# Kernel tuning notes

Measured on AMD Instinct MI355X. Metric: run time of the kernel, lower is better.

## Reference

```python
import jax, jax.numpy as jnp
import numpy as np

N_NODES = 100000
N_EDGES = 1600000
D_IN = 128
UNITS = 128


def setup_inputs() -> dict:
    key = jax.random.key(0)
    k1, k2, k3, k4, k5 = jax.random.split(key, 5)
    x = jax.random.normal(k1, (N_NODES, D_IN), dtype=jnp.float32)
    # glorot-uniform-like dense weight
    limit = float(np.sqrt(6.0 / (D_IN + UNITS)))
    w = jax.random.uniform(k2, (D_IN, UNITS), minval=-limit, maxval=limit, dtype=jnp.float32)
    # COO sparse adjacency: A[row, col] = val
    edge_row = jax.random.randint(k3, (N_EDGES,), 0, N_NODES, dtype=jnp.int32)
    edge_col = jax.random.randint(k4, (N_EDGES,), 0, N_NODES, dtype=jnp.int32)
    edge_val = jax.random.uniform(k5, (N_EDGES,), dtype=jnp.float32)
    return {"x": x, "w": w, "edge_row": edge_row, "edge_col": edge_col, "edge_val": edge_val}


def reference(x, w, edge_row, edge_col, edge_val):
    # dropout rate = 0.0 -> identity (module default)
    xw = x @ w                                   # [N, units] dense projection
    # sparse adjacency propagation: out[i] = sum_e val[e] * xw[col[e]] for row[e]==i
    msgs = xw[edge_col] * edge_val[:, None]      # [E, units] irregular gather
    out = jax.ops.segment_sum(msgs, edge_row, num_segments=x.shape[0])
    return jax.nn.relu(out)                      # activation
```

## Files before the change

kernel.cpp:

```cpp
#include <hip/hip_runtime.h>

#define N_NODES 100000
#define N_EDGES 1600000
#define D 128
#define NB 391
#define BCAP 4608
#define BSTRIDE 16
#define CHUNK 4000
#define NSCAT 400

typedef __attribute__((ext_vector_type(8))) short  short8;
typedef __attribute__((ext_vector_type(4))) float  floatx4;

__device__ __forceinline__ ushort f2bf(float f) {
    unsigned u = __float_as_uint(f);
    u += 0x7FFF + ((u >> 16) & 1);
    return (ushort)(u >> 16);
}
__device__ __forceinline__ float bf2f(ushort s) {
    return __uint_as_float((unsigned)s << 16);
}

__global__ __launch_bounds__(256) void gemm_xw_mfma(const float* __restrict__ x,
                                                    const float* __restrict__ w,
                                                    ushort* __restrict__ xwb) {
    __shared__ ushort wt[128 * 128];
    const int tid  = threadIdx.x;
    const int wv   = tid >> 6;
    const int lane = tid & 63;
    const int m    = lane & 15;
    const int q    = lane >> 4;

    {
        const float4* w4 = (const float4*)w;
        for (int i = tid; i < 4096; i += 256) {
            const float4 v = w4[i];
            const int k = i >> 5;
            const int n = (i & 31) << 2;
            const int c = k >> 3, kc = k & 7;
#pragma unroll
            for (int d = 0; d < 4; ++d) {
                const float val = (d == 0) ? v.x : (d == 1) ? v.y : (d == 2) ? v.z : v.w;
                const int nn = n + d;
                wt[(nn << 7) | (((c ^ (nn & 15)) & 15) << 3) | kc] = f2bf(val);
            }
        }
    }
    __syncthreads();

    const int rbase = blockIdx.x * 64 + wv * 16;
    if (rbase >= N_NODES) return;

    const float* xrow = x + (size_t)(rbase + m) * D;

    floatx4 acc[8];
#pragma unroll
    for (int t = 0; t < 8; ++t) acc[t] = (floatx4){0.f, 0.f, 0.f, 0.f};

#pragma unroll
    for (int kk = 0; kk < D; kk += 32) {
        const float4 a0 = *(const float4*)(xrow + kk + q * 8);
        const float4 a1 = *(const float4*)(xrow + kk + q * 8 + 4);
        short8 a;
        a[0] = (short)f2bf(a0.x); a[1] = (short)f2bf(a0.y);
        a[2] = (short)f2bf(a0.z); a[3] = (short)f2bf(a0.w);
        a[4] = (short)f2bf(a1.x); a[5] = (short)f2bf(a1.y);
        a[6] = (short)f2bf(a1.z); a[7] = (short)f2bf(a1.w);

#pragma unroll
        for (int t = 0; t < 8; ++t) {
            const int n  = t * 16 + m;
            const int cc = (((kk >> 3) + q) ^ m) & 15;
            const short8 b = *(const short8*)&wt[(n << 7) | (cc << 3)];
            acc[t] = __builtin_amdgcn_mfma_f32_16x16x32_bf16(a, b, acc[t], 0, 0, 0);
        }
    }

#pragma unroll
    for (int t = 0; t < 8; ++t) {
#pragma unroll
        for (int r = 0; r < 4; ++r) {
            xwb[(size_t)(rbase + q * 4 + r) * D + t * 16 + m] = f2bf(acc[t][r]);
        }
    }
}

__global__ __launch_bounds__(256) void bucket_scatter(const int* __restrict__ erow,
                                                      const int* __restrict__ ecol,
                                                      const float* __restrict__ eval,
                                                      int* __restrict__ bcnt,
                                                      int2* __restrict__ bkt) {
    __shared__ int  sA[512];
    __shared__ int  sB[512];
    __shared__ int  lcur[NB];
    __shared__ int  gbase[NB];
    __shared__ int2 stage[CHUNK];
    const int t  = threadIdx.x;
    const int e0 = blockIdx.x * CHUNK;

    sA[t] = 0; sA[t + 256] = 0;
    __syncthreads();

    for (int i = t; i < CHUNK; i += 256) {
        const int r = erow[e0 + i];
        atomicAdd(&sA[r >> 8], 1);
    }
    __syncthreads();

    int cur = 0;
    int* bufs[2] = {sA, sB};
#pragma unroll
    for (int o = 1; o < 512; o <<= 1) {
        const int* src = bufs[cur];
        int*       dst = bufs[cur ^ 1];
        const int i0 = t, i1 = t + 256;
        dst[i0] = src[i0] + ((i0 >= o) ? src[i0 - o] : 0);
        dst[i1] = src[i1] + ((i1 >= o) ? src[i1 - o] : 0);
        cur ^= 1;
        __syncthreads();
    }
    {
        const int* incl = bufs[cur];
        int*       excl = bufs[cur ^ 1];
        excl[t]       = (t == 0) ? 0 : incl[t - 1];
        excl[t + 256] = incl[t + 255];
    }
    __syncthreads();
    int* L = bufs[cur ^ 1];

    for (int b = t; b < NB; b += 256) {
        lcur[b] = L[b];
        const int cnt = L[b + 1] - L[b];
        gbase[b] = (cnt > 0) ? atomicAdd(&bcnt[b * BSTRIDE], cnt) : 0;
    }
    __syncthreads();

    for (int i = t; i < CHUNK; i += 256) {
        const int   r = erow[e0 + i];
        const int   c = ecol[e0 + i];
        const float v = eval[e0 + i];
        const int   b = r >> 8;
        const int pos = atomicAdd(&lcur[b], 1);
        stage[pos] = make_int2(((r & 255) << 17) | c, __float_as_int(v));
    }
    __syncthreads();

    for (int i = t; i < CHUNK; i += 256) {
        int lo = 0, hi = NB - 1;
        while (lo < hi) {
            const int mid = (lo + hi + 1) >> 1;
            if (L[mid] <= i) lo = mid; else hi = mid - 1;
        }
        const int b   = lo;
        const int dst = gbase[b] + (i - L[b]);
        if (dst < BCAP) bkt[(size_t)b * BCAP + dst] = stage[i];
    }
}

__global__ __launch_bounds__(512) void scan_partials(const int* __restrict__ bcnt,
                                                     int* __restrict__ part) {
    __shared__ int buf[2][512];
    const int t = threadIdx.x;
    const int v = (t < NB) ? min(bcnt[t * BSTRIDE], BCAP) : 0;
    buf[0][t] = v;
    __syncthreads();
    int cur = 0;
#pragma unroll
    for (int o = 1; o < 512; o <<= 1) {
        const int nv = buf[cur][t] + ((t >= o) ? buf[cur][t - o] : 0);
        buf[cur ^ 1][t] = nv;
        cur ^= 1;
        __syncthreads();
    }
    if (t < NB) part[t] = buf[cur][t] - v;
}

__global__ __launch_bounds__(256) void bucket_to_csr(const int* __restrict__ bcnt,
                                                     const int* __restrict__ part,
                                                     const int2* __restrict__ bkt,
                                                     int* __restrict__ off,
                                                     int2* __restrict__ csr_cv) {
    __shared__ int sA[256], sB[256], lcur[256];
    const int b = blockIdx.x;
    const int t = threadIdx.x;
    const int n = min(bcnt[b * BSTRIDE], BCAP);
    const int2* src = bkt + (size_t)b * BCAP;
    const int base = part[b];

    sA[t] = 0;
    __syncthreads();
    for (int i = t; i < n; i += 256) {
        atomicAdd(&sA[((unsigned)src[i].x) >> 17], 1);
    }
    __syncthreads();
    int cur = 0;
    int* bufs[2] = {sA, sB};
#pragma unroll
    for (int o = 1; o < 256; o <<= 1) {
        const int* s = bufs[cur];
        int*       d = bufs[cur ^ 1];
        d[t] = s[t] + ((t >= o) ? s[t - o] : 0);
        cur ^= 1;
        __syncthreads();
    }
    const int excl = (t == 0) ? 0 : bufs[cur][t - 1];
    const int gr = (b << 8) + t;
    if (gr <= N_NODES) off[gr] = base + excl;
    lcur[t] = base + excl;
    __syncthreads();

    for (int i = t; i < n; i += 256) {
        const int2 e = src[i];
        const int  rl = ((unsigned)e.x) >> 17;
        const int pos = atomicAdd(&lcur[rl], 1);
        csr_cv[pos] = make_int2(e.x & 0x1FFFF, e.y);
    }
}

__global__ __launch_bounds__(256) void gather_kernel(const int* __restrict__ off,
                                                     const int2* __restrict__ csr_cv,
                                                     const ushort* __restrict__ xwb,
                                                     float* __restrict__ out) {
    const int node = blockIdx.x * 4 + (threadIdx.x >> 6);
    const int l    = threadIdx.x & 63;
    if (node >= N_NODES) return;
    const int q  = l >> 4;
    const int lc = (l & 15) << 3;

    int       j   = off[node] + q;
    const int end = off[node + 1];

    float acc0[8] = {0, 0, 0, 0, 0, 0, 0, 0};
    float acc1[8] = {0, 0, 0, 0, 0, 0, 0, 0};

    for (; j + 4 < end; j += 8) {
        const int2 cva = csr_cv[j];
        const int2 cvb = csr_cv[j + 4];
        const short8 ma = *(const short8*)&xwb[(size_t)cva.x * D + lc];
        const short8 mb = *(const short8*)&xwb[(size_t)cvb.x * D + lc];
        const float va = __int_as_float(cva.y);
        const float vb = __int_as_float(cvb.y);
#pragma unroll
        for (int i = 0; i < 8; ++i) {
            acc0[i] += va * bf2f((ushort)ma[i]);
            acc1[i] += vb * bf2f((ushort)mb[i]);
        }
    }
    if (j < end) {
        const int2 cv = csr_cv[j];
        const short8 m = *(const short8*)&xwb[(size_t)cv.x * D + lc];
        const float v = __int_as_float(cv.y);
#pragma unroll
        for (int i = 0; i < 8; ++i) acc0[i] += v * bf2f((ushort)m[i]);
    }

#pragma unroll
    for (int i = 0; i < 8; ++i) {
        float s = acc0[i] + acc1[i];
        s += __shfl_down(s, 32);
        s += __shfl_down(s, 16);
        acc0[i] = fmaxf(s, 0.f);
    }

    if (q == 0) {
        float4 o0 = make_float4(acc0[0], acc0[1], acc0[2], acc0[3]);
        float4 o1 = make_float4(acc0[4], acc0[5], acc0[6], acc0[7]);
        float* o = out + (size_t)node * D + lc;
        *(float4*)(o + 0) = o0;
        *(float4*)(o + 4) = o1;
    }
}

extern "C" void kernel_launch(void* const* d_in, const int* in_sizes, int n_in,
                              void* d_out, int out_size, void* d_ws, size_t ws_size,
                              hipStream_t stream) {
    const float* x    = (const float*)d_in[0];
    const float* w    = (const float*)d_in[1];
    const int*   erow = (const int*)d_in[2];
    const int*   ecol = (const int*)d_in[3];
    const float* eval = (const float*)d_in[4];
    float*       out  = (float*)d_out;

    char*   ws_base = (char*)d_ws;
    ushort* xwb    = (ushort*)ws_base;
    int*    bcnt   = (int*)(ws_base + 25600000);
    int*    off    = (int*)(ws_base + 25625024);
    int*    part   = (int*)(ws_base + 26025040);
    int2*   bkt    = (int2*)(ws_base + 26026608);
    int2*   csr_cv = (int2*)(ws_base + 40440432);

    hipMemsetAsync(bcnt, 0, 25024, stream);

    gemm_xw_mfma<<<(N_NODES + 63) / 64, 256, 0, stream>>>(x, w, xwb);
    bucket_scatter<<<NSCAT, 256, 0, stream>>>(erow, ecol, eval, bcnt, bkt);
    scan_partials<<<1, 512, 0, stream>>>(bcnt, part);
    bucket_to_csr<<<NB, 256, 0, stream>>>(bcnt, part, bkt, off, csr_cv);
    gather_kernel<<<(N_NODES + 3) / 4, 256, 0, stream>>>(off, csr_cv, xwb, out);
}
```

Before: 255.5 us.

## Fuse GEMM with bucket scatter, stage buckets in LDS, widen gather unroll

Merges the GEMM and edge-bucketing kernels into one launch by splitting on block index, so the two independent stages run concurrently and one launch is dropped. The scatter stores each staged element's bucket id instead of binary-searching for it. The CSR-build kernel copies its bucket into LDS once rather than reading global memory twice. The gather loop is unrolled to four independent edges per iteration for more memory-level parallelism, and output stores become nontemporal. The shared-memory union grows LDS per block, which may lower occupancy for the GEMM blocks.

```diff
diff --git a/kernel.cpp b/kernel.cpp
--- a/kernel.cpp
+++ b/kernel.cpp
@@ -8,6 +8,7 @@
 #define BSTRIDE 16
 #define CHUNK 4000
 #define NSCAT 400
+#define NGEMM 1563
 
 typedef __attribute__((ext_vector_type(8))) short  short8;
 typedef __attribute__((ext_vector_type(4))) float  floatx4;
@@ -21,139 +22,149 @@
     return __uint_as_float((unsigned)s << 16);
 }
 
-__global__ __launch_bounds__(256) void gemm_xw_mfma(const float* __restrict__ x,
-                                                    const float* __restrict__ w,
-                                                    ushort* __restrict__ xwb) {
-    __shared__ ushort wt[128 * 128];
-    const int tid  = threadIdx.x;
-    const int wv   = tid >> 6;
-    const int lane = tid & 63;
-    const int m    = lane & 15;
-    const int q    = lane >> 4;
-
-    {
-        const float4* w4 = (const float4*)w;
-        for (int i = tid; i < 4096; i += 256) {
-            const float4 v = w4[i];
-            const int k = i >> 5;
-            const int n = (i & 31) << 2;
-            const int c = k >> 3, kc = k & 7;
-#pragma unroll
-            for (int d = 0; d < 4; ++d) {
-                const float val = (d == 0) ? v.x : (d == 1) ? v.y : (d == 2) ? v.z : v.w;
-                const int nn = n + d;
-                wt[(nn << 7) | (((c ^ (nn & 15)) & 15) << 3) | kc] = f2bf(val);
+union SMem {
+    struct {
+        int2  stage[CHUNK];
+        int   sA[512];
+        int   sB[512];
+        int   lcur[NB];
+        int   gbase[NB];
+        short sbuck[CHUNK];
+    } sc;
+    ushort wt[128 * 128];
+};
+
+__global__ __launch_bounds__(256) void gemm_and_scatter(const float* __restrict__ x,
+                                                        const float* __restrict__ w,
+                                                        ushort* __restrict__ xwb,
+                                                        const int* __restrict__ erow,
+                                                        const int* __restrict__ ecol,
+                                                        const float* __restrict__ eval,
+                                                        int* __restrict__ bcnt,
+                                                        int2* __restrict__ bkt) {
+    __shared__ SMem sm;
+    const int t = threadIdx.x;
+
+    if (blockIdx.x < NGEMM) {
+        ushort* wt = sm.wt;
+        const int wv   = t >> 6;
+        const int lane = t & 63;
+        const int m    = lane & 15;
+        const int q    = lane >> 4;
+
+        {
+            const float4* w4 = (const float4*)w;
+            for (int i = t; i < 4096; i += 256) {
+                const float4 v = w4[i];
+                const int k = i >> 5;
+                const int n = (i & 31) << 2;
+                const int c = k >> 3, kc = k & 7;
+#pragma unroll
+                for (int d = 0; d < 4; ++d) {
+                    const float val = (d == 0) ? v.x : (d == 1) ? v.y : (d == 2) ? v.z : v.w;
+                    const int nn = n + d;
+                    wt[(nn << 7) | (((c ^ (nn & 15)) & 15) << 3) | kc] = f2bf(val);
+                }
             }
         }
-    }
-    __syncthreads();
-
-    const int rbase = blockIdx.x * 64 + wv * 16;
-    if (rbase >= N_NODES) return;
-
-    const float* xrow = x + (size_t)(rbase + m) * D;
-
-    floatx4 acc[8];
-#pragma unroll
-    for (int t = 0; t < 8; ++t) acc[t] = (floatx4){0.f, 0.f, 0.f, 0.f};
-
-#pragma unroll
-    for (int kk = 0; kk < D; kk += 32) {
-        const float4 a0 = *(const float4*)(xrow + kk + q * 8);
-        const float4 a1 = *(const float4*)(xrow + kk + q * 8 + 4);
-        short8 a;
-        a[0] = (short)f2bf(a0.x); a[1] = (short)f2bf(a0.y);
-        a[2] = (short)f2bf(a0.z); a[3] = (short)f2bf(a0.w);
-        a[4] = (short)f2bf(a1.x); a[5] = (short)f2bf(a1.y);
-        a[6] = (short)f2bf(a1.z); a[7] = (short)f2bf(a1.w);
-
-#pragma unroll
-        for (int t = 0; t < 8; ++t) {
-            const int n  = t * 16 + m;
-            const int cc = (((kk >> 3) + q) ^ m) & 15;
-            const short8 b = *(const short8*)&wt[(n << 7) | (cc << 3)];
-            acc[t] = __builtin_amdgcn_mfma_f32_16x16x32_bf16(a, b, acc[t], 0, 0, 0);
-        }
-    }
-
-#pragma unroll
-    for (int t = 0; t < 8; ++t) {
-#pragma unroll
-        for (int r = 0; r < 4; ++r) {
-            xwb[(size_t)(rbase + q * 4 + r) * D + t * 16 + m] = f2bf(acc[t][r]);
-        }
-    }
-}
-
-__global__ __launch_bounds__(256) void bucket_scatter(const int* __restrict__ erow,
-                                                      const int* __restrict__ ecol,
-                                                      const float* __restrict__ eval,
-                                                      int* __restrict__ bcnt,
-                                                      int2* __restrict__ bkt) {
-    __shared__ int  sA[512];
-    __shared__ int  sB[512];
-    __shared__ int  lcur[NB];
-    __shared__ int  gbase[NB];
-    __shared__ int2 stage[CHUNK];
-    const int t  = threadIdx.x;
-    const int e0 = blockIdx.x * CHUNK;
-
-    sA[t] = 0; sA[t + 256] = 0;
-    __syncthreads();
-
-    for (int i = t; i < CHUNK; i += 256) {
-        const int r = erow[e0 + i];
-        atomicAdd(&sA[r >> 8], 1);
-    }
-    __syncthreads();
-
-    int cur = 0;
-    int* bufs[2] = {sA, sB};
-#pragma unroll
-    for (int o = 1; o < 512; o <<= 1) {
-        const int* src = bufs[cur];
-        int*       dst = bufs[cur ^ 1];
-        const int i0 = t, i1 = t + 256;
-        dst[i0] = src[i0] + ((i0 >= o) ? src[i0 - o] : 0);
-        dst[i1] = src[i1] + ((i1 >= o) ? src[i1 - o] : 0);
-        cur ^= 1;
-        __syncthreads();
-    }
-    {
-        const int* incl = bufs[cur];
-        int*       excl = bufs[cur ^ 1];
-        excl[t]       = (t == 0) ? 0 : incl[t - 1];
-        excl[t + 256] = incl[t + 255];
-    }
-    __syncthreads();
-    int* L = bufs[cur ^ 1];
-
-    for (int b = t; b < NB; b += 256) {
-        lcur[b] = L[b];
-        const int cnt = L[b + 1] - L[b];
-        gbase[b] = (cnt > 0) ? atomicAdd(&bcnt[b * BSTRIDE], cnt) : 0;
-    }
-    __syncthreads();
-
-    for (int i = t; i < CHUNK; i += 256) {
-        const int   r = erow[e0 + i];
-        const int   c = ecol[e0 + i];
-        const float v = eval[e0 + i];
-        const int   b = r >> 8;
-        const int pos = atomicAdd(&lcur[b], 1);
-        stage[pos] = make_int2(((r & 255) << 17) | c, __float_as_int(v));
-    }
-    __syncthreads();
-
-    for (int i = t; i < CHUNK; i += 256) {
-        int lo = 0, hi = NB - 1;
-        while (lo < hi) {
-            const int mid = (lo + hi + 1) >> 1;
-            if (L[mid] <= i) lo = mid; else hi = mid - 1;
-        }
-        const int b   = lo;
-        const int dst = gbase[b] + (i - L[b]);
-        if (dst < BCAP) bkt[(size_t)b * BCAP + dst] = stage[i];
+        __syncthreads();
+
+        const int rbase = blockIdx.x * 64 + wv * 16;
+        if (rbase >= N_NODES) return;
+
+        const float* xrow = x + (size_t)(rbase + m) * D;
+
+        floatx4 acc[8];
+#pragma unroll
+        for (int tt = 0; tt < 8; ++tt) acc[tt] = (floatx4){0.f, 0.f, 0.f, 0.f};
+
+#pragma unroll
+        for (int kk = 0; kk < D; kk += 32) {
+            const float4 a0 = *(const float4*)(xrow + kk + q * 8);
+            const float4 a1 = *(const float4*)(xrow + kk + q * 8 + 4);
+            short8 a;
+            a[0] = (short)f2bf(a0.x); a[1] = (short)f2bf(a0.y);
+            a[2] = (short)f2bf(a0.z); a[3] = (short)f2bf(a0.w);
+            a[4] = (short)f2bf(a1.x); a[5] = (short)f2bf(a1.y);
+            a[6] = (short)f2bf(a1.z); a[7] = (short)f2bf(a1.w);
+
+#pragma unroll
+            for (int tt = 0; tt < 8; ++tt) {
+                const int n  = tt * 16 + m;
+                const int cc = (((kk >> 3) + q) ^ m) & 15;
+                const short8 b = *(const short8*)&wt[(n << 7) | (cc << 3)];
+                acc[tt] = __builtin_amdgcn_mfma_f32_16x16x32_bf16(a, b, acc[tt], 0, 0, 0);
+            }
+        }
+
+#pragma unroll
+        for (int tt = 0; tt < 8; ++tt) {
+#pragma unroll
+            for (int r = 0; r < 4; ++r) {
+                xwb[(size_t)(rbase + q * 4 + r) * D + tt * 16 + m] = f2bf(acc[tt][r]);
+            }
+        }
+    } else {
+        const int e0 = (blockIdx.x - NGEMM) * CHUNK;
+        int*   sA    = sm.sc.sA;
+        int*   sB    = sm.sc.sB;
+        int*   lcur  = sm.sc.lcur;
+        int*   gbase = sm.sc.gbase;
+        short* sbuck = sm.sc.sbuck;
+        int2*  stage = sm.sc.stage;
+
+        sA[t] = 0; sA[t + 256] = 0;
+        __syncthreads();
+
+        for (int i = t; i < CHUNK; i += 256) {
+            atomicAdd(&sA[erow[e0 + i] >> 8], 1);
+        }
+        __syncthreads();
+
+        int cur = 0;
+        int* bufs[2] = {sA, sB};
+#pragma unroll
+        for (int o = 1; o < 512; o <<= 1) {
+            const int* src = bufs[cur];
+            int*       dst = bufs[cur ^ 1];
+            const int i0 = t, i1 = t + 256;
+            dst[i0] = src[i0] + ((i0 >= o) ? src[i0 - o] : 0);
+            dst[i1] = src[i1] + ((i1 >= o) ? src[i1 - o] : 0);
+            cur ^= 1;
+            __syncthreads();
+        }
+        {
+            const int* incl = bufs[cur];
+            int*       excl = bufs[cur ^ 1];
+            excl[t]       = (t == 0) ? 0 : incl[t - 1];
+            excl[t + 256] = incl[t + 255];
+        }
+        __syncthreads();
+        int* L = bufs[cur ^ 1];
+
+        for (int b = t; b < NB; b += 256) {
+            lcur[b] = L[b];
+            const int cnt = L[b + 1] - L[b];
+            gbase[b] = (cnt > 0) ? atomicAdd(&bcnt[b * BSTRIDE], cnt) : 0;
+        }
+        __syncthreads();
+
+        for (int i = t; i < CHUNK; i += 256) {
+            const int   r = erow[e0 + i];
+            const int   c = ecol[e0 + i];
+            const float v = eval[e0 + i];
+            const int   b = r >> 8;
+            const int pos = atomicAdd(&lcur[b], 1);
+            stage[pos] = make_int2(((r & 255) << 17) | c, __float_as_int(v));
+            sbuck[pos] = (short)b;
+        }
+        __syncthreads();
+
+        for (int i = t; i < CHUNK; i += 256) {
+            const int b   = sbuck[i];
+            const int dst = gbase[b] + (i - L[b]);
+            if (dst < BCAP) bkt[(size_t)b * BCAP + dst] = stage[i];
+        }
     }
 }
 
@@ -180,19 +191,23 @@
                                                      const int2* __restrict__ bkt,
                                                      int* __restrict__ off,
                                                      int2* __restrict__ csr_cv) {
-    __shared__ int sA[256], sB[256], lcur[256];
+    __shared__ int2 stage[BCAP];
+    __shared__ int  sA[256], sB[256], lcur[256];
     const int b = blockIdx.x;
     const int t = threadIdx.x;
     const int n = min(bcnt[b * BSTRIDE], BCAP);
     const int2* src = bkt + (size_t)b * BCAP;
     const int base = part[b];
 
+    for (int i = t; i < n; i += 256) stage[i] = src[i];
     sA[t] = 0;
     __syncthreads();
+
     for (int i = t; i < n; i += 256) {
-        atomicAdd(&sA[((unsigned)src[i].x) >> 17], 1);
+        atomicAdd(&sA[((unsigned)stage[i].x) >> 17], 1);
     }
     __syncthreads();
+
     int cur = 0;
     int* bufs[2] = {sA, sB};
 #pragma unroll
@@ -210,7 +225,7 @@
     __syncthreads();
 
     for (int i = t; i < n; i += 256) {
-        const int2 e = src[i];
+        const int2 e = stage[i];
         const int  rl = ((unsigned)e.x) >> 17;
         const int pos = atomicAdd(&lcur[rl], 1);
         csr_cv[pos] = make_int2(e.x & 0x1FFFF, e.y);
@@ -232,21 +247,31 @@
 
     float acc0[8] = {0, 0, 0, 0, 0, 0, 0, 0};
     float acc1[8] = {0, 0, 0, 0, 0, 0, 0, 0};
-
-    for (; j + 4 < end; j += 8) {
+    float acc2[8] = {0, 0, 0, 0, 0, 0, 0, 0};
+    float acc3[8] = {0, 0, 0, 0, 0, 0, 0, 0};
+
+    for (; j + 12 < end; j += 16) {
         const int2 cva = csr_cv[j];
         const int2 cvb = csr_cv[j + 4];
+        const int2 cvc = csr_cv[j + 8];
+        const int2 cvd = csr_cv[j + 12];
         const short8 ma = *(const short8*)&xwb[(size_t)cva.x * D + lc];
         const short8 mb = *(const short8*)&xwb[(size_t)cvb.x * D + lc];
+        const short8 mc = *(const short8*)&xwb[(size_t)cvc.x * D + lc];
+        const short8 md = *(const short8*)&xwb[(size_t)cvd.x * D + lc];
         const float va = __int_as_float(cva.y);
         const float vb = __int_as_float(cvb.y);
+        const float vc = __int_as_float(cvc.y);
+        const float vd = __int_as_float(cvd.y);
 #pragma unroll
         for (int i = 0; i < 8; ++i) {
             acc0[i] += va * bf2f((ushort)ma[i]);
             acc1[i] += vb * bf2f((ushort)mb[i]);
-        }
-    }
-    if (j < end) {
+            acc2[i] += vc * bf2f((ushort)mc[i]);
+            acc3[i] += vd * bf2f((ushort)md[i]);
+        }
+    }
+    for (; j < end; j += 4) {
         const int2 cv = csr_cv[j];
         const short8 m = *(const short8*)&xwb[(size_t)cv.x * D + lc];
         const float v = __int_as_float(cv.y);
@@ -256,18 +281,18 @@
 
 #pragma unroll
     for (int i = 0; i < 8; ++i) {
-        float s = acc0[i] + acc1[i];
+        float s = (acc0[i] + acc1[i]) + (acc2[i] + acc3[i]);
         s += __shfl_down(s, 32);
         s += __shfl_down(s, 16);
         acc0[i] = fmaxf(s, 0.f);
     }
 
     if (q == 0) {
-        float4 o0 = make_float4(acc0[0], acc0[1], acc0[2], acc0[3]);
-        float4 o1 = make_float4(acc0[4], acc0[5], acc0[6], acc0[7]);
+        floatx4 o0 = {acc0[0], acc0[1], acc0[2], acc0[3]};
+        floatx4 o1 = {acc0[4], acc0[5], acc0[6], acc0[7]};
         float* o = out + (size_t)node * D + lc;
-        *(float4*)(o + 0) = o0;
-        *(float4*)(o + 4) = o1;
+        __builtin_nontemporal_store(o0, (floatx4*)(o + 0));
+        __builtin_nontemporal_store(o1, (floatx4*)(o + 4));
     }
 }
 
@@ -289,10 +314,9 @@
     int2*   bkt    = (int2*)(ws_base + 26026608);
     int2*   csr_cv = (int2*)(ws_base + 40440432);
 
-    hipMemsetAsync(bcnt, 0, 25024, stream);
-
-    gemm_xw_mfma<<<(N_NODES + 63) / 64, 256, 0, stream>>>(x, w, xwb);
-    bucket_scatter<<<NSCAT, 256, 0, stream>>>(erow, ecol, eval, bcnt, bkt);
+    (void)hipMemsetAsync(bcnt, 0, 25024, stream);
+
+    gemm_and_scatter<<<NGEMM + NSCAT, 256, 0, stream>>>(x, w, xwb, erow, ecol, eval, bcnt, bkt);
     scan_partials<<<1, 512, 0, stream>>>(bcnt, part);
     bucket_to_csr<<<NB, 256, 0, stream>>>(bcnt, part, bkt, off, csr_cv);
     gather_kernel<<<(N_NODES + 3) / 4, 256, 0, stream>>>(off, csr_cv, xwb, out);
```

New measurement: 255.5 us. Within noise of the previous version (+0.0%).
